# Kernel tuning notes

Measured on AMD Instinct MI355X. Metric: run time of the kernel, lower is better.

The kernel has to match this reference:

```python
import jax, jax.numpy as jnp
import numpy as np

N_NODES = 100000
N_EDGES = 1600000
N_GRAPHS = 64
EMB_DIM = 64
DIMS = [6, 16, 32, 64, EMB_DIM]


def setup_inputs() -> dict:
    key = jax.random.key(0)
    ks = jax.random.split(key, 16)
    feat = jax.random.normal(ks[0], (N_NODES, DIMS[0]), dtype=jnp.float32)
    src = jax.random.randint(ks[1], (N_EDGES,), 0, N_NODES)
    dst = jax.random.randint(ks[2], (N_EDGES,), 0, N_NODES)
    graph_ids = jnp.sort(jax.random.randint(ks[3], (N_NODES,), 0, N_GRAPHS))
    inp = {"feat": feat, "src": src, "dst": dst, "graph_ids": graph_ids}
    # fc_neigh weights for each SAGEConv (gcn aggregator has no fc_self), Xavier-ish init
    for i in range(4):
        din, dout = DIMS[i], DIMS[i + 1]
        scale = 1.0 / np.sqrt(din)
        inp[f"W{i+1}"] = jax.random.uniform(ks[4 + 2 * i], (din, dout), jnp.float32, -scale, scale)
        inp[f"b{i+1}"] = jnp.zeros((dout,), jnp.float32)
    return inp


def _sage_gcn(feat, src, dst, deg, W, b):
    # DGL SAGEConv aggregator_type='gcn':
    # h_neigh = (sum_{u in N(v)} h_u + h_v) / (in_deg(v) + 1); out = h_neigh @ W + b
    neigh = jax.ops.segment_sum(feat[src], dst, num_segments=N_NODES)  # [N, din]
    h = (neigh + feat) / (deg[:, None] + 1.0)
    return h @ W + b


def reference(feat, src, dst, graph_ids, W1, b1, W2, b2, W3, b3, W4, b4):
    deg = jax.ops.segment_sum(jnp.ones((N_EDGES,), feat.dtype), dst, num_segments=N_NODES)
    h = feat
    for W, b in ((W1, b1), (W2, b2), (W3, b3), (W4, b4)):
        h = jax.nn.relu(_sage_gcn(h, src, dst, deg, W, b))
    # dgl.mean_nodes: per-graph mean over nodes
    sums = jax.ops.segment_sum(h, graph_ids, num_segments=N_GRAPHS)          # [G, emb]
    cnts = jax.ops.segment_sum(jnp.ones((N_NODES,), h.dtype), graph_ids, num_segments=N_GRAPHS)
    return sums / jnp.maximum(cnts, 1.0)[:, None]
```

## Files before the change

### kernel.cpp

```cpp
#include <hip/hip_runtime.h>
#include <hip/hip_bf16.h>
#include <hip/hip_fp16.h>

#define N_NODES 100000
#define N_EDGES 1600000
#define N_GRAPHS 64

#define NB_BKT 256
#define NPBKT 391
#define EPB 2048
#define NBLK_BIN ((N_EDGES + EPB - 1) / EPB)


__device__ __forceinline__ __half2 u2h(unsigned int u) {
    return __builtin_bit_cast(__half2, u);
}
__device__ __forceinline__ float2 u2f2(unsigned int u) {
    return __half22float2(u2h(u));
}
__device__ __forceinline__ unsigned int packh2(float a, float b) {
    return __builtin_bit_cast(unsigned int, __float22half2_rn(make_float2(a, b)));
}


__global__ __launch_bounds__(256) void bin_count(const int* __restrict__ dst,
                                                 int* __restrict__ cntmat, int E) {
    __shared__ int cnt[NB_BKT];
    int t = threadIdx.x;
    int e0 = blockIdx.x * EPB;
    cnt[t] = 0;
    __syncthreads();
#pragma unroll
    for (int k = 0; k < 8; ++k) {
        int e = e0 + k * 256 + t;
        if (e < E) {
            unsigned d = (unsigned)dst[e];
            atomicAdd(&cnt[d / (unsigned)NPBKT], 1);
        }
    }
    __syncthreads();
    cntmat[(size_t)blockIdx.x * NB_BKT + t] = cnt[t];
}

__global__ __launch_bounds__(256) void bin_scan(int* __restrict__ cntmat,
                                                int* __restrict__ gcnt, int nblk) {
    __shared__ int s[256];
    int b = blockIdx.x, t = threadIdx.x;
    int running = 0;
    for (int c0 = 0; c0 < nblk; c0 += 256) {
        int idx = c0 + t;
        int v = (idx < nblk) ? cntmat[(size_t)idx * NB_BKT + b] : 0;
        s[t] = v;
        __syncthreads();
        for (int o = 1; o < 256; o <<= 1) {
            int a = (t >= o) ? s[t - o] : 0;
            __syncthreads();
            s[t] += a;
            __syncthreads();
        }
        if (idx < nblk) cntmat[(size_t)idx * NB_BKT + b] = running + s[t] - v;
        running += s[255];
        __syncthreads();
    }
    if (t == 0) gcnt[b] = running;
}

__global__ __launch_bounds__(256) void bin_write(const int* __restrict__ dst,
                                                 const int* __restrict__ src,
                                                 const int* __restrict__ cntmat,
                                                 const int* __restrict__ gcnt,
                                                 uint2* __restrict__ rec, int E) {
    __shared__ int cnt[NB_BKT];
    __shared__ int lbase[NB_BKT];
    __shared__ int gofs[NB_BKT];
    __shared__ uint2 stage[EPB];
    int t = threadIdx.x;
    int e0 = blockIdx.x * EPB;
    int g = gcnt[t];
    lbase[t] = g;
    __syncthreads();
    for (int o = 1; o < 256; o <<= 1) {
        int a = (t >= o) ? lbase[t - o] : 0;
        __syncthreads();
        lbase[t] += a;
        __syncthreads();
    }
    gofs[t] = (lbase[t] - g) + cntmat[(size_t)blockIdx.x * NB_BKT + t];
    cnt[t] = 0;
    __syncthreads();
    int myb[8], mypos[8];
    unsigned myd[8], mys[8];
#pragma unroll
    for (int k = 0; k < 8; ++k) {
        int e = e0 + k * 256 + t;
        if (e < E) {
            unsigned d = (unsigned)dst[e];
            int b = (int)(d / (unsigned)NPBKT);
            myd[k] = d;
            mys[k] = (unsigned)src[e];
            myb[k] = b;
            mypos[k] = atomicAdd(&cnt[b], 1);
        } else {
            myb[k] = -1;
        }
    }
    __syncthreads();
    int c = cnt[t];
    lbase[t] = c;
    __syncthreads();
    for (int o = 1; o < 256; o <<= 1) {
        int a = (t >= o) ? lbase[t - o] : 0;
        __syncthreads();
        lbase[t] += a;
        __syncthreads();
    }
    lbase[t] = lbase[t] - c;
    __syncthreads();
#pragma unroll
    for (int k = 0; k < 8; ++k)
        if (myb[k] >= 0) stage[lbase[myb[k]] + mypos[k]] = make_uint2(myd[k], mys[k]);
    __syncthreads();
    int total = min(EPB, E - e0);
    for (int i = t; i < total; i += 256) {
        int lo = 0, hi = NB_BKT - 1;
        while (lo < hi) {
            int m = (lo + hi + 1) >> 1;
            if (lbase[m] <= i) lo = m; else hi = m - 1;
        }
        rec[(size_t)gofs[lo] + (i - lbase[lo])] = stage[i];
    }
}

__global__ __launch_bounds__(256) void fill_bucket(const uint2* __restrict__ rec,
                                                   const int* __restrict__ gcnt,
                                                   int* __restrict__ rp,
                                                   int* __restrict__ col, int n) {
    __shared__ int sdeg[512];
    __shared__ int lcur[512];
    __shared__ int sg[256];
    __shared__ int lcol[8192];
    int p = blockIdx.x, t = threadIdx.x;
    int nbase = p * NPBKT;
    int nn = min(NPBKT, n - nbase);
    int g = gcnt[t];
    sg[t] = g;
    __syncthreads();
    for (int o = 1; o < 256; o <<= 1) {
        int a = (t >= o) ? sg[t - o] : 0;
        __syncthreads();
        sg[t] += a;
        __syncthreads();
    }
    int ex = sg[t] - g;
    __syncthreads();
    sg[t] = ex;
    __syncthreads();
    int cbase = sg[p];
    int cnt = gcnt[p];
    sdeg[t] = 0;
    sdeg[t + 256] = 0;
    __syncthreads();
    const uint2* r = rec + cbase;
    for (int i = t; i < cnt; i += 256) atomicAdd(&sdeg[r[i].x - (unsigned)nbase], 1);
    __syncthreads();
    int c0 = sdeg[t], c1 = sdeg[t + 256];
    for (int o = 1; o < 512; o <<= 1) {
        int a = (t >= o) ? sdeg[t - o] : 0;
        int b = (t + 256 >= o) ? sdeg[t + 256 - o] : 0;
        __syncthreads();
        sdeg[t] += a;
        sdeg[t + 256] += b;
        __syncthreads();
    }
    int ex0 = sdeg[t] - c0, ex1 = sdeg[t + 256] - c1;
    lcur[t] = ex0;
    lcur[t + 256] = ex1;
    if (t < nn) rp[nbase + t] = cbase + ex0;
    if (t + 256 < nn) rp[nbase + t + 256] = cbase + ex1;
    if (p == NB_BKT - 1 && t == 0) rp[n] = cbase + cnt;
    __syncthreads();
    for (int i = t; i < cnt; i += 256) {
        uint2 e = r[i];
        int slot = atomicAdd(&lcur[e.x - (unsigned)nbase], 1);
        lcol[slot] = (int)e.y;
    }
    __syncthreads();
    for (int i = t; i < cnt; i += 256) col[cbase + i] = lcol[i];
}


__global__ __launch_bounds__(256) void sage_layer1(const float* __restrict__ feat,
                                                   const int* __restrict__ rp,
                                                   const int* __restrict__ col,
                                                   const float* __restrict__ W,
                                                   const float* __restrict__ bias,
                                                   unsigned int* __restrict__ hout, int n) {
    __shared__ float sW[6 * 16];
    __shared__ float sB[16];
    int tid = threadIdx.x;
    if (tid < 96) sW[tid] = W[tid];
    if (tid < 16) sB[tid] = bias[tid];
    __syncthreads();
    int v = blockIdx.x * 256 + tid;
    if (v >= n) return;
    int r0 = rp[v], r1 = rp[v + 1];
    float acc[6] = {0.f, 0.f, 0.f, 0.f, 0.f, 0.f};
    const float2* f2 = reinterpret_cast<const float2*>(feat);
    int j = r0;
    for (; j + 4 <= r1; j += 4) {
        int u0 = col[j], u1 = col[j + 1], u2 = col[j + 2], u3 = col[j + 3];
        float2 a0 = f2[u0 * 3 + 0], b0 = f2[u0 * 3 + 1], c0 = f2[u0 * 3 + 2];
        float2 a1 = f2[u1 * 3 + 0], b1 = f2[u1 * 3 + 1], c1 = f2[u1 * 3 + 2];
        float2 a2 = f2[u2 * 3 + 0], b2 = f2[u2 * 3 + 1], c2 = f2[u2 * 3 + 2];
        float2 a3 = f2[u3 * 3 + 0], b3 = f2[u3 * 3 + 1], c3 = f2[u3 * 3 + 2];
        acc[0] += (a0.x + a1.x) + (a2.x + a3.x);
        acc[1] += (a0.y + a1.y) + (a2.y + a3.y);
        acc[2] += (b0.x + b1.x) + (b2.x + b3.x);
        acc[3] += (b0.y + b1.y) + (b2.y + b3.y);
        acc[4] += (c0.x + c1.x) + (c2.x + c3.x);
        acc[5] += (c0.y + c1.y) + (c2.y + c3.y);
    }
    for (; j < r1; ++j) {
        int u = col[j];
        float2 a = f2[u * 3 + 0], b = f2[u * 3 + 1], c = f2[u * 3 + 2];
        acc[0] += a.x; acc[1] += a.y;
        acc[2] += b.x; acc[3] += b.y;
        acc[4] += c.x; acc[5] += c.y;
    }
    {
        float2 a = f2[v * 3 + 0], b = f2[v * 3 + 1], c = f2[v * 3 + 2];
        acc[0] += a.x; acc[1] += a.y;
        acc[2] += b.x; acc[3] += b.y;
        acc[4] += c.x; acc[5] += c.y;
    }
    float inv = 1.0f / (float)(r1 - r0 + 1);
#pragma unroll
    for (int k = 0; k < 6; ++k) acc[k] *= inv;
    float outv[16];
#pragma unroll
    for (int o = 0; o < 16; ++o) outv[o] = sB[o];
#pragma unroll
    for (int k = 0; k < 6; ++k) {
#pragma unroll
        for (int o = 0; o < 16; ++o) outv[o] += acc[k] * sW[k * 16 + o];
    }
    unsigned int w[8];
#pragma unroll
    for (int o = 0; o < 16; o += 2)
        w[o / 2] = packh2(fmaxf(outv[o], 0.f), fmaxf(outv[o + 1], 0.f));
    uint4* op = reinterpret_cast<uint4*>(hout + v * 8);
    op[0] = make_uint4(w[0], w[1], w[2], w[3]);
    op[1] = make_uint4(w[4], w[5], w[6], w[7]);
}


template <int DIN, int DOUT>
__global__ __launch_bounds__(256) void sage_f16(const uint4* __restrict__ hin,
                                                const int* __restrict__ rp,
                                                const int* __restrict__ col,
                                                const float* __restrict__ W,
                                                const float* __restrict__ bias,
                                                unsigned int* __restrict__ hout, int n) {
    constexpr int WPN = DIN / 8;
    constexpr int NPB = 256 / WPN;
    constexpr int OPT = DOUT / WPN;
    __shared__ float sW[DIN * DOUT];
    __shared__ float sB[DOUT];
    __shared__ float sH[NPB][DIN + 1];

    int tid = threadIdx.x;
    for (int i = tid; i < DIN * DOUT; i += 256) sW[i] = W[i];
    if (tid < DOUT) sB[tid] = bias[tid];

    int sub = tid / WPN;
    int t = tid % WPN;
    int v = blockIdx.x * NPB + sub;

    if (v < n) {
        int r0 = rp[v], r1 = rp[v + 1];
        const __half2 z = __float2half2_rn(0.f);
        __half2 acc[4][4];
#pragma unroll
        for (int s = 0; s < 4; ++s)
#pragma unroll
            for (int q = 0; q < 4; ++q) acc[s][q] = z;
        int j = r0;
        for (; j + 8 <= r1; j += 8) {
            uint4 w[8];
#pragma unroll
            for (int k = 0; k < 8; ++k) w[k] = hin[col[j + k] * WPN + t];
#pragma unroll
            for (int k = 0; k < 8; ++k) {
                __half2* a = acc[k & 3];
                a[0] = __hadd2(a[0], u2h(w[k].x));
                a[1] = __hadd2(a[1], u2h(w[k].y));
                a[2] = __hadd2(a[2], u2h(w[k].z));
                a[3] = __hadd2(a[3], u2h(w[k].w));
            }
        }
        for (; j + 4 <= r1; j += 4) {
            uint4 w[4];
#pragma unroll
            for (int k = 0; k < 4; ++k) w[k] = hin[col[j + k] * WPN + t];
#pragma unroll
            for (int k = 0; k < 4; ++k) {
                __half2* a = acc[k];
                a[0] = __hadd2(a[0], u2h(w[k].x));
                a[1] = __hadd2(a[1], u2h(w[k].y));
                a[2] = __hadd2(a[2], u2h(w[k].z));
                a[3] = __hadd2(a[3], u2h(w[k].w));
            }
        }
        for (; j < r1; ++j) {
            uint4 w = hin[col[j] * WPN + t];
            acc[0][0] = __hadd2(acc[0][0], u2h(w.x));
            acc[0][1] = __hadd2(acc[0][1], u2h(w.y));
            acc[0][2] = __hadd2(acc[0][2], u2h(w.z));
            acc[0][3] = __hadd2(acc[0][3], u2h(w.w));
        }
#pragma unroll
        for (int q = 0; q < 4; ++q)
            acc[0][q] = __hadd2(__hadd2(acc[0][q], acc[1][q]),
                                __hadd2(acc[2][q], acc[3][q]));
        uint4 ws = hin[v * WPN + t];
        unsigned swd[4] = {ws.x, ws.y, ws.z, ws.w};
        float inv = 1.0f / (float)(r1 - r0 + 1);
#pragma unroll
        for (int q = 0; q < 4; ++q) {
            float2 f = __half22float2(acc[0][q]);
            float2 s = u2f2(swd[q]);
            sH[sub][t * 8 + 2 * q + 0] = (f.x + s.x) * inv;
            sH[sub][t * 8 + 2 * q + 1] = (f.y + s.y) * inv;
        }
    }
    __syncthreads();
    if (v < n) {
        int o0 = t * OPT;
        float accO[OPT];
#pragma unroll
        for (int i = 0; i < OPT; ++i) accO[i] = sB[o0 + i];
#pragma unroll 4
        for (int k = 0; k < DIN; ++k) {
            float hk = sH[sub][k];
#pragma unroll
            for (int i = 0; i < OPT; ++i) accO[i] += hk * sW[k * DOUT + o0 + i];
        }
        unsigned wds[OPT / 2];
#pragma unroll
        for (int i = 0; i < OPT; i += 2)
            wds[i / 2] = packh2(fmaxf(accO[i], 0.f), fmaxf(accO[i + 1], 0.f));
        unsigned* op = hout + v * (DOUT / 2) + o0 / 2;
        if constexpr (OPT / 2 == 4) {
            *reinterpret_cast<uint4*>(op) = make_uint4(wds[0], wds[1], wds[2], wds[3]);
        } else if constexpr (OPT / 2 == 8) {
            reinterpret_cast<uint4*>(op)[0] = make_uint4(wds[0], wds[1], wds[2], wds[3]);
            reinterpret_cast<uint4*>(op)[1] = make_uint4(wds[4], wds[5], wds[6], wds[7]);
        } else {
            *reinterpret_cast<uint2*>(op) = make_uint2(wds[0], wds[1]);
        }
    }
}


__device__ __forceinline__ int lower_bound_i(const int* __restrict__ a, int n, int key) {
    int lo = 0, hi = n;
    while (lo < hi) {
        int m = (lo + hi) >> 1;
        if (a[m] < key) lo = m + 1; else hi = m;
    }
    return lo;
}

__global__ __launch_bounds__(256) void pool_f16(const unsigned int* __restrict__ h32,
                                                const int* __restrict__ gids,
                                                float* __restrict__ out, int n) {
    int bx = blockIdx.x;
    int g = bx >> 3, s = bx & 7;
    int start = lower_bound_i(gids, n, g);
    int end = lower_bound_i(gids, n, g + 1);
    int len = end - start;
    float inv = 1.0f / (float)(len > 0 ? len : 1);
    int chunk = (len + 7) / 8;
    int s0 = start + s * chunk;
    int s1 = min(s0 + chunk, end);
    int t = threadIdx.x;
    int d = t & 31, j = t >> 5;
    float a0 = 0.f, a1 = 0.f;
    for (int i = s0 + j; i < s1; i += 8) {
        float2 f = u2f2(h32[(size_t)i * 32 + d]);
        a0 += f.x;
        a1 += f.y;
    }
    __shared__ float red[8][32][2];
    red[j][d][0] = a0;
    red[j][d][1] = a1;
    __syncthreads();
    if (t < 64) {
        int dd = t & 31, e = t >> 5;
        float tot = 0.f;
#pragma unroll
        for (int k = 0; k < 8; ++k) tot += red[k][dd][e];
        atomicAdd(&out[g * 64 + 2 * dd + e], tot * inv);
    }
}


extern "C" void kernel_launch(void* const* d_in, const int* in_sizes, int n_in,
                              void* d_out, int out_size, void* d_ws, size_t ws_size,
                              hipStream_t stream) {
    const int N = N_NODES, E = N_EDGES;
    const float* feat = (const float*)d_in[0];
    const int* src = (const int*)d_in[1];
    const int* dst = (const int*)d_in[2];
    const int* gids = (const int*)d_in[3];
    const float* W1 = (const float*)d_in[4];
    const float* b1 = (const float*)d_in[5];
    const float* W2 = (const float*)d_in[6];
    const float* b2 = (const float*)d_in[7];
    const float* W3 = (const float*)d_in[8];
    const float* b3 = (const float*)d_in[9];
    const float* W4 = (const float*)d_in[10];
    const float* b4 = (const float*)d_in[11];
    float* out = (float*)d_out;

    int* rp = (int*)d_ws;
    int* gcnt = rp + (N + 1);
    int* cntmat = gcnt + 256;
    int* col = cntmat + (size_t)NBLK_BIN * 256;
    size_t off = (size_t)((char*)(col + E) - (char*)d_ws);
    off = (off + 255) & ~(size_t)255;
    unsigned int* h1 = (unsigned int*)((char*)d_ws + off);
    unsigned int* h2 = h1 + (size_t)N * 8;
    unsigned int* h3 = h2 + (size_t)N * 16;
    unsigned int* h4 = h3 + (size_t)N * 32;
    uint2* rec = (uint2*)h3;

    hipMemsetAsync(out, 0, (size_t)N_GRAPHS * 64 * sizeof(float), stream);

    bin_count<<<NBLK_BIN, 256, 0, stream>>>(dst, cntmat, E);
    bin_scan<<<NB_BKT, 256, 0, stream>>>(cntmat, gcnt, NBLK_BIN);
    bin_write<<<NBLK_BIN, 256, 0, stream>>>(dst, src, cntmat, gcnt, rec, E);
    fill_bucket<<<NB_BKT, 256, 0, stream>>>(rec, gcnt, rp, col, N);

    sage_layer1<<<(N + 255) / 256, 256, 0, stream>>>(feat, rp, col, W1, b1, h1, N);
    sage_f16<16, 32><<<(N + 127) / 128, 256, 0, stream>>>(
        (const uint4*)h1, rp, col, W2, b2, h2, N);
    sage_f16<32, 64><<<(N + 63) / 64, 256, 0, stream>>>(
        (const uint4*)h2, rp, col, W3, b3, h3, N);
    sage_f16<64, 64><<<(N + 31) / 32, 256, 0, stream>>>(
        (const uint4*)h3, rp, col, W4, b4, h4, N);

    pool_f16<<<N_GRAPHS * 8, 256, 0, stream>>>(h4, gids, out, N);
}
```

Baseline: 176.8 us.

## Fuse mean pooling into last layer, fp16 layer-1 input, larger bin blocks

Converts the 6-wide fp32 input features into padded fp16 rows so layer 1 can reuse the generic fp16 gather kernel instead of a dedicated fp32 one. The last layer now accumulates its ReLU outputs straight into per-graph shared-memory sums and atomically adds them to the output, with a small finalize kernel dividing by node counts. This drops the h4 write/read and the separate pooling pass. The edge binning kernels also process 4096 edges per block instead of 2048, halving the block count at the cost of more registers per thread. Layer-1 inputs lose precision when rounded to fp16, and the pooled sums now rely on many global atomics.

```diff
diff --git a/kernel.cpp b/kernel.cpp
--- a/kernel.cpp
+++ b/kernel.cpp
@@ -8,7 +8,7 @@
 
 #define NB_BKT 256
 #define NPBKT 391
-#define EPB 2048
+#define EPB 4096
 #define NBLK_BIN ((N_EDGES + EPB - 1) / EPB)
 
 
@@ -20,6 +20,27 @@
 }
 __device__ __forceinline__ unsigned int packh2(float a, float b) {
     return __builtin_bit_cast(unsigned int, __float22half2_rn(make_float2(a, b)));
+}
+
+
+__global__ __launch_bounds__(256) void feat_to_h8(const float* __restrict__ feat,
+                                                  uint4* __restrict__ out, int n) {
+    __shared__ float s[256 * 6];
+    int b0 = blockIdx.x * 256;
+    int t = threadIdx.x;
+    int cnt = (min(256, n - b0)) * 6;
+    for (int i = t; i < cnt; i += 256) s[i] = feat[(size_t)b0 * 6 + i];
+    __syncthreads();
+    int v = b0 + t;
+    if (v < n) {
+        const float* f = s + t * 6;
+        uint4 r;
+        r.x = packh2(f[0], f[1]);
+        r.y = packh2(f[2], f[3]);
+        r.z = packh2(f[4], f[5]);
+        r.w = 0u;
+        out[v] = r;
+    }
 }
 
 
@@ -31,7 +52,7 @@
     cnt[t] = 0;
     __syncthreads();
 #pragma unroll
-    for (int k = 0; k < 8; ++k) {
+    for (int k = 0; k < 16; ++k) {
         int e = e0 + k * 256 + t;
         if (e < E) {
             unsigned d = (unsigned)dst[e];
@@ -88,10 +109,10 @@
     gofs[t] = (lbase[t] - g) + cntmat[(size_t)blockIdx.x * NB_BKT + t];
     cnt[t] = 0;
     __syncthreads();
-    int myb[8], mypos[8];
-    unsigned myd[8], mys[8];
-#pragma unroll
-    for (int k = 0; k < 8; ++k) {
+    int myb[16], mypos[16];
+    unsigned myd[16], mys[16];
+#pragma unroll
+    for (int k = 0; k < 16; ++k) {
         int e = e0 + k * 256 + t;
         if (e < E) {
             unsigned d = (unsigned)dst[e];
@@ -117,7 +138,7 @@
     lbase[t] = lbase[t] - c;
     __syncthreads();
 #pragma unroll
-    for (int k = 0; k < 8; ++k)
+    for (int k = 0; k < 16; ++k)
         if (myb[k] >= 0) stage[lbase[myb[k]] + mypos[k]] = make_uint2(myd[k], mys[k]);
     __syncthreads();
     int total = min(EPB, E - e0);
@@ -189,88 +210,40 @@
 }
 
 
-__global__ __launch_bounds__(256) void sage_layer1(const float* __restrict__ feat,
-                                                   const int* __restrict__ rp,
-                                                   const int* __restrict__ col,
-                                                   const float* __restrict__ W,
-                                                   const float* __restrict__ bias,
-                                                   unsigned int* __restrict__ hout, int n) {
-    __shared__ float sW[6 * 16];
-    __shared__ float sB[16];
-    int tid = threadIdx.x;
-    if (tid < 96) sW[tid] = W[tid];
-    if (tid < 16) sB[tid] = bias[tid];
-    __syncthreads();
-    int v = blockIdx.x * 256 + tid;
-    if (v >= n) return;
-    int r0 = rp[v], r1 = rp[v + 1];
-    float acc[6] = {0.f, 0.f, 0.f, 0.f, 0.f, 0.f};
-    const float2* f2 = reinterpret_cast<const float2*>(feat);
-    int j = r0;
-    for (; j + 4 <= r1; j += 4) {
-        int u0 = col[j], u1 = col[j + 1], u2 = col[j + 2], u3 = col[j + 3];
-        float2 a0 = f2[u0 * 3 + 0], b0 = f2[u0 * 3 + 1], c0 = f2[u0 * 3 + 2];
-        float2 a1 = f2[u1 * 3 + 0], b1 = f2[u1 * 3 + 1], c1 = f2[u1 * 3 + 2];
-        float2 a2 = f2[u2 * 3 + 0], b2 = f2[u2 * 3 + 1], c2 = f2[u2 * 3 + 2];
-        float2 a3 = f2[u3 * 3 + 0], b3 = f2[u3 * 3 + 1], c3 = f2[u3 * 3 + 2];
-        acc[0] += (a0.x + a1.x) + (a2.x + a3.x);
-        acc[1] += (a0.y + a1.y) + (a2.y + a3.y);
-        acc[2] += (b0.x + b1.x) + (b2.x + b3.x);
-        acc[3] += (b0.y + b1.y) + (b2.y + b3.y);
-        acc[4] += (c0.x + c1.x) + (c2.x + c3.x);
-        acc[5] += (c0.y + c1.y) + (c2.y + c3.y);
-    }
-    for (; j < r1; ++j) {
-        int u = col[j];
-        float2 a = f2[u * 3 + 0], b = f2[u * 3 + 1], c = f2[u * 3 + 2];
-        acc[0] += a.x; acc[1] += a.y;
-        acc[2] += b.x; acc[3] += b.y;
-        acc[4] += c.x; acc[5] += c.y;
-    }
-    {
-        float2 a = f2[v * 3 + 0], b = f2[v * 3 + 1], c = f2[v * 3 + 2];
-        acc[0] += a.x; acc[1] += a.y;
-        acc[2] += b.x; acc[3] += b.y;
-        acc[4] += c.x; acc[5] += c.y;
-    }
-    float inv = 1.0f / (float)(r1 - r0 + 1);
-#pragma unroll
-    for (int k = 0; k < 6; ++k) acc[k] *= inv;
-    float outv[16];
-#pragma unroll
-    for (int o = 0; o < 16; ++o) outv[o] = sB[o];
-#pragma unroll
-    for (int k = 0; k < 6; ++k) {
-#pragma unroll
-        for (int o = 0; o < 16; ++o) outv[o] += acc[k] * sW[k * 16 + o];
-    }
-    unsigned int w[8];
-#pragma unroll
-    for (int o = 0; o < 16; o += 2)
-        w[o / 2] = packh2(fmaxf(outv[o], 0.f), fmaxf(outv[o + 1], 0.f));
-    uint4* op = reinterpret_cast<uint4*>(hout + v * 8);
-    op[0] = make_uint4(w[0], w[1], w[2], w[3]);
-    op[1] = make_uint4(w[4], w[5], w[6], w[7]);
-}
-
-
-template <int DIN, int DOUT>
+__device__ __forceinline__ int lower_bound_i(const int* __restrict__ a, int n, int key) {
+    int lo = 0, hi = n;
+    while (lo < hi) {
+        int m = (lo + hi) >> 1;
+        if (a[m] < key) lo = m + 1; else hi = m;
+    }
+    return lo;
+}
+
+template <int DIN, int DOUT, bool POOL>
 __global__ __launch_bounds__(256) void sage_f16(const uint4* __restrict__ hin,
                                                 const int* __restrict__ rp,
                                                 const int* __restrict__ col,
                                                 const float* __restrict__ W,
                                                 const float* __restrict__ bias,
-                                                unsigned int* __restrict__ hout, int n) {
+                                                unsigned int* __restrict__ hout,
+                                                const int* __restrict__ gids,
+                                                float* __restrict__ pout,
+                                                int real_din, int n) {
     constexpr int WPN = DIN / 8;
     constexpr int NPB = 256 / WPN;
     constexpr int OPT = DOUT / WPN;
+    constexpr int PG = POOL ? (NPB + 1) : 1;
     __shared__ float sW[DIN * DOUT];
     __shared__ float sB[DOUT];
     __shared__ float sH[NPB][DIN + 1];
+    __shared__ float spool[PG][64];
 
     int tid = threadIdx.x;
-    for (int i = tid; i < DIN * DOUT; i += 256) sW[i] = W[i];
+    for (int i = tid; i < DIN * DOUT; i += 256) sW[i] = (i < real_din * DOUT) ? W[i] : 0.f;
     if (tid < DOUT) sB[tid] = bias[tid];
+    if constexpr (POOL) {
+        for (int i = tid; i < PG * 64; i += 256) (&spool[0][0])[i] = 0.f;
+    }
 
     int sub = tid / WPN;
     int t = tid % WPN;
@@ -345,62 +318,57 @@
 #pragma unroll
             for (int i = 0; i < OPT; ++i) accO[i] += hk * sW[k * DOUT + o0 + i];
         }
-        unsigned wds[OPT / 2];
-#pragma unroll
-        for (int i = 0; i < OPT; i += 2)
-            wds[i / 2] = packh2(fmaxf(accO[i], 0.f), fmaxf(accO[i + 1], 0.f));
-        unsigned* op = hout + v * (DOUT / 2) + o0 / 2;
-        if constexpr (OPT / 2 == 4) {
-            *reinterpret_cast<uint4*>(op) = make_uint4(wds[0], wds[1], wds[2], wds[3]);
-        } else if constexpr (OPT / 2 == 8) {
-            reinterpret_cast<uint4*>(op)[0] = make_uint4(wds[0], wds[1], wds[2], wds[3]);
-            reinterpret_cast<uint4*>(op)[1] = make_uint4(wds[4], wds[5], wds[6], wds[7]);
+        if constexpr (POOL) {
+            int g0 = gids[blockIdx.x * NPB];
+            int gi = gids[v] - g0;
+            gi = (gi < PG) ? gi : (PG - 1);
+#pragma unroll
+            for (int i = 0; i < OPT; ++i)
+                atomicAdd(&spool[gi][o0 + i], fmaxf(accO[i], 0.f));
         } else {
-            *reinterpret_cast<uint2*>(op) = make_uint2(wds[0], wds[1]);
-        }
-    }
-}
-
-
-__device__ __forceinline__ int lower_bound_i(const int* __restrict__ a, int n, int key) {
-    int lo = 0, hi = n;
-    while (lo < hi) {
-        int m = (lo + hi) >> 1;
-        if (a[m] < key) lo = m + 1; else hi = m;
-    }
-    return lo;
-}
-
-__global__ __launch_bounds__(256) void pool_f16(const unsigned int* __restrict__ h32,
-                                                const int* __restrict__ gids,
-                                                float* __restrict__ out, int n) {
-    int bx = blockIdx.x;
-    int g = bx >> 3, s = bx & 7;
-    int start = lower_bound_i(gids, n, g);
-    int end = lower_bound_i(gids, n, g + 1);
-    int len = end - start;
-    float inv = 1.0f / (float)(len > 0 ? len : 1);
-    int chunk = (len + 7) / 8;
-    int s0 = start + s * chunk;
-    int s1 = min(s0 + chunk, end);
+            unsigned wds[OPT / 2];
+#pragma unroll
+            for (int i = 0; i < OPT; i += 2)
+                wds[i / 2] = packh2(fmaxf(accO[i], 0.f), fmaxf(accO[i + 1], 0.f));
+            unsigned* op = hout + v * (DOUT / 2) + o0 / 2;
+            if constexpr (OPT / 2 == 4) {
+                *reinterpret_cast<uint4*>(op) = make_uint4(wds[0], wds[1], wds[2], wds[3]);
+            } else if constexpr (OPT / 2 == 8) {
+                reinterpret_cast<uint4*>(op)[0] = make_uint4(wds[0], wds[1], wds[2], wds[3]);
+                reinterpret_cast<uint4*>(op)[1] = make_uint4(wds[4], wds[5], wds[6], wds[7]);
+            } else {
+                *reinterpret_cast<uint2*>(op) = make_uint2(wds[0], wds[1]);
+            }
+        }
+    }
+    if constexpr (POOL) {
+        __syncthreads();
+        int v0 = blockIdx.x * NPB;
+        if (v0 < n) {
+            int g0 = gids[v0];
+            int glast = gids[min(v0 + NPB - 1, n - 1)];
+            int ngr = glast - g0 + 1;
+            ngr = (ngr < PG) ? ngr : PG;
+            int tot = ngr * 64;
+            for (int i = tid; i < tot; i += 256)
+                atomicAdd(&pout[(g0 + (i >> 6)) * 64 + (i & 63)], spool[i >> 6][i & 63]);
+        }
+    }
+}
+
+__global__ __launch_bounds__(256) void finalize_pool(const int* __restrict__ gids,
+                                                     float* __restrict__ out, int n) {
+    __shared__ int cnts[N_GRAPHS];
     int t = threadIdx.x;
-    int d = t & 31, j = t >> 5;
-    float a0 = 0.f, a1 = 0.f;
-    for (int i = s0 + j; i < s1; i += 8) {
-        float2 f = u2f2(h32[(size_t)i * 32 + d]);
-        a0 += f.x;
-        a1 += f.y;
-    }
-    __shared__ float red[8][32][2];
-    red[j][d][0] = a0;
-    red[j][d][1] = a1;
-    __syncthreads();
-    if (t < 64) {
-        int dd = t & 31, e = t >> 5;
-        float tot = 0.f;
-#pragma unroll
-        for (int k = 0; k < 8; ++k) tot += red[k][dd][e];
-        atomicAdd(&out[g * 64 + 2 * dd + e], tot * inv);
+    if (t < N_GRAPHS) {
+        int s = lower_bound_i(gids, n, t);
+        int e = lower_bound_i(gids, n, t + 1);
+        cnts[t] = e - s;
+    }
+    __syncthreads();
+    for (int i = t; i < N_GRAPHS * 64; i += 256) {
+        int c = cnts[i >> 6];
+        out[i] *= 1.0f / (float)(c > 0 ? c : 1);
     }
 }
 
@@ -432,23 +400,25 @@
     unsigned int* h1 = (unsigned int*)((char*)d_ws + off);
     unsigned int* h2 = h1 + (size_t)N * 8;
     unsigned int* h3 = h2 + (size_t)N * 16;
-    unsigned int* h4 = h3 + (size_t)N * 32;
+    uint4* feat16 = (uint4*)(h3 + (size_t)N * 32);
     uint2* rec = (uint2*)h3;
 
     hipMemsetAsync(out, 0, (size_t)N_GRAPHS * 64 * sizeof(float), stream);
 
+    feat_to_h8<<<(N + 255) / 256, 256, 0, stream>>>(feat, feat16, N);
     bin_count<<<NBLK_BIN, 256, 0, stream>>>(dst, cntmat, E);
     bin_scan<<<NB_BKT, 256, 0, stream>>>(cntmat, gcnt, NBLK_BIN);
     bin_write<<<NBLK_BIN, 256, 0, stream>>>(dst, src, cntmat, gcnt, rec, E);
     fill_bucket<<<NB_BKT, 256, 0, stream>>>(rec, gcnt, rp, col, N);
 
-    sage_layer1<<<(N + 255) / 256, 256, 0, stream>>>(feat, rp, col, W1, b1, h1, N);
-    sage_f16<16, 32><<<(N + 127) / 128, 256, 0, stream>>>(
-        (const uint4*)h1, rp, col, W2, b2, h2, N);
-    sage_f16<32, 64><<<(N + 63) / 64, 256, 0, stream>>>(
-        (const uint4*)h2, rp, col, W3, b3, h3, N);
-    sage_f16<64, 64><<<(N + 31) / 32, 256, 0, stream>>>(
-        (const uint4*)h3, rp, col, W4, b4, h4, N);
-
-    pool_f16<<<N_GRAPHS * 8, 256, 0, stream>>>(h4, gids, out, N);
-}
+    sage_f16<8, 16, false><<<(N + 255) / 256, 256, 0, stream>>>(
+        feat16, rp, col, W1, b1, h1, nullptr, nullptr, 6, N);
+    sage_f16<16, 32, false><<<(N + 127) / 128, 256, 0, stream>>>(
+        (const uint4*)h1, rp, col, W2, b2, h2, nullptr, nullptr, 16, N);
+    sage_f16<32, 64, false><<<(N + 63) / 64, 256, 0, stream>>>(
+        (const uint4*)h2, rp, col, W3, b3, h3, nullptr, nullptr, 32, N);
+    sage_f16<64, 64, true><<<(N + 31) / 32, 256, 0, stream>>>(
+        (const uint4*)h3, rp, col, W4, b4, nullptr, gids, out, 64, N);
+
+    finalize_pool<<<1, 256, 0, stream>>>(gids, out, N);
+}
```

New measurement: 219.7 us. 1.24x slower.
